# Performance work log

Hardware: AMD Instinct MI355X
Metric: run time of the kernel (lower is better)

The kernel has to match this reference:

```python
import jax, jax.numpy as jnp
import numpy as np
from jax import lax

B, CEN, CDE, H, W = 4, 256, 256, 64, 64   # de is (B,CDE,H,W); en is (B,CEN,2H,2W)
EMB, K, SCALE = 64, 5, 2
DN = ('NCHW', 'OIHW', 'NCHW')


def conv2d(x, w, b=None, pad=0):
    y = lax.conv_general_dilated(x, w, (1, 1), [(pad, pad), (pad, pad)], dimension_numbers=DN)
    return y if b is None else y + b[None, :, None, None]


def up2(x):
    # F.interpolate(scale_factor=2) default mode='nearest'
    return jnp.repeat(jnp.repeat(x, 2, axis=2), 2, axis=3)


def carafe(de, kernels, k, scale):
    # de: (B,C,H,W); kernels: (B,k*k,H*scale,W*scale), softmax-normalized over dim 1
    b, c, h, w = de.shape
    pad = k // 2
    dep = jnp.pad(de, ((0, 0), (0, 0), (pad, pad), (pad, pad)))
    # (B, C, k*k, H, W): all k*k shifted views of de (zero-padded borders)
    patches = jnp.stack([dep[:, :, dy:dy + h, dx:dx + w]
                         for dy in range(k) for dx in range(k)], axis=2)
    # each output pixel (i,j) reuses the window at source (i//scale, j//scale)
    ker = kernels.reshape(b, k * k, h, scale, w, scale)
    out = jnp.einsum('bkhxwy,bckhw->bchxwy', ker, patches)
    return out.reshape(b, c, h * scale, w * scale)


def xavier_uniform(key, shape):
    fan_out = shape[0] * shape[2] * shape[3]
    fan_in = shape[1] * shape[2] * shape[3]
    limit = float(np.sqrt(6.0 / (fan_in + fan_out)))
    return jax.random.uniform(key, shape, jnp.float32, -limit, limit)


def setup_inputs() -> dict:
    key = jax.random.key(0)
    ks = jax.random.split(key, 7)
    return {
        'en': jax.random.normal(ks[0], (B, CEN, 2 * H, 2 * W), jnp.float32),
        'de': jax.random.normal(ks[1], (B, CDE, H, W), jnp.float32),
        'w_gate': xavier_uniform(ks[2], (1, CDE, 1, 1)),
        'b_gate': jnp.zeros((1,), jnp.float32),
        'w_cen': xavier_uniform(ks[3], (EMB, CEN, 1, 1)),
        'b_cen': jnp.zeros((EMB,), jnp.float32),
        'w_cde': xavier_uniform(ks[4], (EMB, CDE, 1, 1)),
        'w_ce': xavier_uniform(ks[5], (K * K, EMB, 3, 3)),
        'b_ce': jnp.zeros((K * K,), jnp.float32),
    }


def reference(en, de, w_gate, b_gate, w_cen, b_cen, w_cde, w_ce, b_ce):
    # GateGenerator: sigmoid(interpolate(conv1x1(de), x2))
    gate = jax.nn.sigmoid(up2(conv2d(de, w_gate, b_gate)))
    # SemiShift: shared 3x3 content encoder on compressed en and upsampled compressed de
    enc = conv2d(en, w_cen, b_cen)
    dec = conv2d(de, w_cde)          # no bias
    logits = conv2d(enc, w_ce, b_ce, pad=1) + up2(conv2d(dec, w_ce, b_ce, pad=1))
    kernels = jax.nn.softmax(logits, axis=1)
    return gate * en + (1.0 - gate) * carafe(de, kernels, K, SCALE)
```

## Files before the change

### kernel.cpp

```cpp
#include <hip/hip_runtime.h>
#include <math.h>

#define BB 4
#define C 256
#define H 64
#define W 64
#define HW 4096
#define HO 128
#define WO 128
#define HWO 16384
#define EMB 64

typedef __bf16 bf16x8 __attribute__((ext_vector_type(8)));
typedef __bf16 bf16x4 __attribute__((ext_vector_type(4)));
typedef float  f32x4  __attribute__((ext_vector_type(4)));

__device__ __forceinline__ f32x4 mfma16(bf16x8 a, bf16x8 b, f32x4 c) {
    return __builtin_amdgcn_mfma_f32_16x16x32_bf16(a, b, c, 0, 0, 0);
}

__global__ void k_prep2(const float* __restrict__ w_cen,
                        const float* __restrict__ w_cde,
                        const float* __restrict__ w_ce,
                        __bf16* __restrict__ wbf_cen,
                        __bf16* __restrict__ wbf_cde,
                        __bf16* __restrict__ w3) {
    const int n1 = EMB * C;
    const int n3 = 9 * 2 * 16 * EMB;
    for (int idx = blockIdx.x * blockDim.x + threadIdx.x; idx < n1;
         idx += gridDim.x * blockDim.x) {
        wbf_cen[idx] = (__bf16)w_cen[idx];
        wbf_cde[idx] = (__bf16)w_cde[idx];
    }
    for (int idx = blockIdx.x * blockDim.x + threadIdx.x; idx < n3;
         idx += gridDim.x * blockDim.x) {
        int e = idx & 63;
        int m = (idx >> 6) & 15;
        int mt = (idx >> 10) & 1;
        int tap = idx >> 11;
        int q = mt * 16 + m;
        int dy = tap / 3, dx = tap % 3;
        w3[idx] = (q < 25) ? (__bf16)w_ce[((q * EMB + e) * 3 + dy) * 3 + dx]
                           : (__bf16)0.0f;
    }
}

__global__ __launch_bounds__(256) void k_gemm1(
        const float* __restrict__ en, const float* __restrict__ de,
        const __bf16* __restrict__ wbf_cen, const __bf16* __restrict__ wbf_cde,
        const float* __restrict__ b_cen,
        __bf16* __restrict__ enc_t, __bf16* __restrict__ dec_t) {
    int t = threadIdx.x;
    int w = t >> 6, lane = t & 63;
    int n = lane & 15, q = lane >> 4;
    bool isenc = blockIdx.x < 512;
    const float* X; const __bf16* Wt; __bf16* Y; int plane, px0;
    if (isenc) {
        int blk = blockIdx.x; int b = blk >> 7; px0 = (blk & 127) << 7;
        X = en + (size_t)b * C * HWO; plane = HWO; Wt = wbf_cen;
        Y = enc_t + (size_t)b * HWO * EMB;
    } else {
        int blk = blockIdx.x - 512; int b = blk >> 5; px0 = (blk & 31) << 7;
        X = de + (size_t)b * C * HW; plane = HW; Wt = wbf_cde;
        Y = dec_t + (size_t)b * HW * EMB;
    }
    int pxw = px0 + w * 32;
    f32x4 acc[4][2] = {};
    for (int kc = 0; kc < 8; kc++) {
        int c0 = kc * 32;
        bf16x8 af[4];
        #pragma unroll
        for (int mt = 0; mt < 4; mt++)
            af[mt] = *(const bf16x8*)(Wt + (mt * 16 + n) * C + c0 + q * 8);
        #pragma unroll
        for (int nt = 0; nt < 2; nt++) {
            int px = pxw + nt * 16 + n;
            bf16x8 bv;
            #pragma unroll
            for (int j = 0; j < 8; j++)
                bv[j] = (__bf16)X[(size_t)(c0 + q * 8 + j) * plane + px];
            #pragma unroll
            for (int mt = 0; mt < 4; mt++)
                acc[mt][nt] = mfma16(af[mt], bv, acc[mt][nt]);
        }
    }
    #pragma unroll
    for (int mt = 0; mt < 4; mt++) {
        int e0 = mt * 16 + q * 4;
        float bias[4];
        #pragma unroll
        for (int r = 0; r < 4; r++) bias[r] = isenc ? b_cen[e0 + r] : 0.f;
        #pragma unroll
        for (int nt = 0; nt < 2; nt++) {
            int px = pxw + nt * 16 + n;
            bf16x4 ov;
            #pragma unroll
            for (int r = 0; r < 4; r++)
                ov[r] = (__bf16)(acc[mt][nt][r] + bias[r]);
            *(bf16x4*)(Y + (size_t)px * EMB + e0) = ov;
        }
    }
}

__global__ __launch_bounds__(256) void k_gate(
        const float* __restrict__ de, const float* __restrict__ w_gate,
        const float* __restrict__ b_gate, float* __restrict__ gate_lr) {
    __shared__ float red[4][64];
    int t = threadIdx.x;
    int px = t & 63, cs = t >> 6;
    int b = blockIdx.x >> 6, p0 = (blockIdx.x & 63) * 64;
    const float* dptr = de + ((size_t)b * C + cs * 64) * HW + p0 + px;
    float s = 0.f;
    #pragma unroll 4
    for (int c = 0; c < 64; c++)
        s += dptr[(size_t)c * HW] * w_gate[cs * 64 + c];
    red[cs][px] = s;
    __syncthreads();
    if (t < 64) {
        float v = red[0][t] + red[1][t] + red[2][t] + red[3][t] + b_gate[0];
        gate_lr[b * HW + p0 + t] = 1.f / (1.f + __expf(-v));
    }
}

__global__ __launch_bounds__(256) void k_conv3m(
        const __bf16* __restrict__ enc_t, const __bf16* __restrict__ dec_t,
        const __bf16* __restrict__ w3, const float* __restrict__ b_ce,
        float* __restrict__ tmp1, float* __restrict__ tmp2) {
    int t = threadIdx.x;
    int w = t >> 6, lane = t & 63;
    int n = lane & 15, q = lane >> 4;
    bool hi = blockIdx.x < 1024;
    const __bf16* src; float* dst; int b, y, width, plane, x;
    if (hi) {
        int blk = blockIdx.x; b = blk >> 8; int r = blk & 255;
        y = r >> 1; int seg = r & 1;
        width = WO; plane = HWO;
        src = enc_t + (size_t)b * HWO * EMB; dst = tmp1;
        x = seg * 64 + w * 16 + n;
    } else {
        int blk = blockIdx.x - 1024; b = blk >> 6; y = blk & 63;
        width = W; plane = HW;
        src = dec_t + (size_t)b * HW * EMB; dst = tmp2;
        x = w * 16 + n;
    }
    f32x4 acc[2] = {};
    bf16x8 bz;
    #pragma unroll
    for (int j = 0; j < 8; j++) bz[j] = (__bf16)0.0f;
    #pragma unroll
    for (int dy = -1; dy <= 1; dy++) {
        int yy = y + dy;
        if ((unsigned)yy >= (unsigned)width) continue;
        #pragma unroll
        for (int dx = -1; dx <= 1; dx++) {
            int tap = (dy + 1) * 3 + (dx + 1);
            int xx = x + dx;
            bool valid = (unsigned)xx < (unsigned)width;
            int xc = valid ? xx : 0;
            const __bf16* brow = src + ((size_t)yy * width + xc) * EMB;
            #pragma unroll
            for (int kc = 0; kc < 2; kc++) {
                bf16x8 bv = *(const bf16x8*)(brow + kc * 32 + q * 8);
                if (!valid) bv = bz;
                #pragma unroll
                for (int mt = 0; mt < 2; mt++) {
                    bf16x8 av = *(const bf16x8*)(
                        w3 + ((tap * 2 + mt) * 16 + n) * EMB + kc * 32 + q * 8);
                    acc[mt] = mfma16(av, bv, acc[mt]);
                }
            }
        }
    }
    #pragma unroll
    for (int mt = 0; mt < 2; mt++) {
        #pragma unroll
        for (int r = 0; r < 4; r++) {
            int m = mt * 16 + q * 4 + r;
            if (m < 25)
                dst[((size_t)(b * 25 + m)) * plane + y * width + x] =
                    acc[mt][r] + b_ce[m];
        }
    }
}

__global__ __launch_bounds__(256) void k_softmax(
        const float* __restrict__ tmp1, const float* __restrict__ tmp2,
        float* __restrict__ kbuf) {
    int gid = blockIdx.x * 256 + threadIdx.x;
    int b = gid >> 14, p = gid & 16383;
    int i = p >> 7, j = p & 127;
    int pl = (i >> 1) * W + (j >> 1);
    float kern[28];
    float m = -1e30f;
    #pragma unroll
    for (int q = 0; q < 25; q++) {
        float l = tmp1[((size_t)(b * 25 + q) << 14) + p]
                + tmp2[((size_t)(b * 25 + q) << 12) + pl];
        kern[q] = l;
        m = fmaxf(m, l);
    }
    float s = 0.f;
    #pragma unroll
    for (int q = 0; q < 25; q++) { kern[q] = __expf(kern[q] - m); s += kern[q]; }
    float inv = 1.f / s;
    #pragma unroll
    for (int q = 0; q < 25; q++) kern[q] *= inv;
    kern[25] = kern[26] = kern[27] = 0.f;
    float4* o = (float4*)(kbuf + (size_t)gid * 28);
    #pragma unroll
    for (int q = 0; q < 7; q++) o[q] = ((float4*)kern)[q];
}

#define NCH 16
__global__ __launch_bounds__(256) void k_final(
        const float* __restrict__ en, const float* __restrict__ de,
        const float* __restrict__ kbuf, const float* __restrict__ gate_lr,
        float* __restrict__ out) {
    __shared__ float sde[NCH][6][36];
    int t = threadIdx.x;
    int tx = t & 63, ty = t >> 6;
    int tileX = blockIdx.x & 1;
    int tileY = blockIdx.x >> 1;
    int c0 = blockIdx.y * NCH;
    int b = blockIdx.z;
    int i0 = tileY * 4, j0 = tileX * 64;
    int yl0 = i0 >> 1, xl0 = j0 >> 1;

    const float* dbase = de + ((size_t)b * C + c0) * HW;
    for (int idx = t; idx < NCH * 216; idx += 256) {
        int c = idx / 216, r = idx % 216;
        int y = r / 36, x = r % 36;
        int yy = yl0 - 2 + y, xx = xl0 - 2 + x;
        float v = 0.f;
        if ((unsigned)yy < (unsigned)H && (unsigned)xx < (unsigned)W)
            v = dbase[(size_t)c * HW + yy * W + xx];
        ((float*)sde)[idx] = v;
    }

    int i = i0 + ty, j = j0 + tx;
    int p = i * WO + j;
    float kern[28];
    const float4* kb = (const float4*)(kbuf + ((size_t)(b * HWO + p)) * 28);
    #pragma unroll
    for (int q = 0; q < 7; q++) ((float4*)kern)[q] = kb[q];
    float g = gate_lr[b * HW + (i >> 1) * W + (j >> 1)];
    __syncthreads();

    int wy = ty >> 1, wx = tx >> 1;
    const float* ebase = en + ((size_t)b * C + c0) * HWO + p;
    float* obase = out + ((size_t)b * C + c0) * HWO + p;
    #pragma unroll 2
    for (int c = 0; c < NCH; c++) {
        float acc = 0.f;
        #pragma unroll
        for (int dy = 0; dy < 5; dy++) {
            #pragma unroll
            for (int dx = 0; dx < 5; dx++)
                acc += kern[dy * 5 + dx] * sde[c][wy + dy][wx + dx];
        }
        float ev = ebase[(size_t)c * HWO];
        obase[(size_t)c * HWO] = g * ev + (1.f - g) * acc;
    }
}

extern "C" void kernel_launch(void* const* d_in, const int* in_sizes, int n_in,
                              void* d_out, int out_size, void* d_ws, size_t ws_size,
                              hipStream_t stream) {
    const float* en     = (const float*)d_in[0];
    const float* de     = (const float*)d_in[1];
    const float* w_gate = (const float*)d_in[2];
    const float* b_gate = (const float*)d_in[3];
    const float* w_cen  = (const float*)d_in[4];
    const float* b_cen  = (const float*)d_in[5];
    const float* w_cde  = (const float*)d_in[6];
    const float* w_ce   = (const float*)d_in[7];
    const float* b_ce   = (const float*)d_in[8];
    float* out = (float*)d_out;

    __bf16* wsb    = (__bf16*)d_ws;
    __bf16* wbf_cen = wsb;
    __bf16* wbf_cde = wbf_cen + 16384;
    __bf16* w3      = wbf_cde + 16384;
    __bf16* enc_t   = w3 + 18432;
    __bf16* dec_t   = enc_t + 4194304;
    float* wsf     = (float*)((char*)d_ws + (size_t)(16384 + 16384 + 18432
                              + 4194304 + 1048576) * 2);
    float* tmp1    = wsf;
    float* tmp2    = tmp1 + 1638400;
    float* gate_lr = tmp2 + 409600;
    float* kbuf    = gate_lr + 16384;

    k_prep2<<<72, 256, 0, stream>>>(w_cen, w_cde, w_ce, wbf_cen, wbf_cde, w3);
    k_gemm1<<<640, 256, 0, stream>>>(en, de, wbf_cen, wbf_cde, b_cen, enc_t, dec_t);
    k_gate<<<256, 256, 0, stream>>>(de, w_gate, b_gate, gate_lr);
    k_conv3m<<<1280, 256, 0, stream>>>(enc_t, dec_t, w3, b_ce, tmp1, tmp2);
    k_softmax<<<256, 256, 0, stream>>>(tmp1, tmp2, kbuf);
    k_final<<<dim3(64, 16, 4), 256, 0, stream>>>(en, de, kbuf, gate_lr, out);
}
```

Measured before the change: 240.0 us.

## Fuse gate into de GEMM, stage conv/GEMM inputs in LDS, retile CARAFE output

The separate gate kernel is removed: the gate 1x1 conv becomes a fifth MFMA row tile in the de projection GEMM, which saves one pass over de. The GEMM now stages input tiles through LDS with float4 loads instead of strided scalar global reads. The 3x3 conv stages a halo of rows in LDS. Softmax splits the 25 taps across four threads per pixel to get more parallelism. The final CARAFE kernel has each thread compute the 2x2 output pixels that share one low-res window, so each shared-memory read serves four outputs, at the cost of more registers.

```diff
diff --git a/kernel.cpp b/kernel.cpp
--- a/kernel.cpp
+++ b/kernel.cpp
@@ -21,18 +21,23 @@
 
 __global__ void k_prep2(const float* __restrict__ w_cen,
                         const float* __restrict__ w_cde,
+                        const float* __restrict__ w_gate,
                         const float* __restrict__ w_ce,
                         __bf16* __restrict__ wbf_cen,
-                        __bf16* __restrict__ wbf_cde,
+                        __bf16* __restrict__ wdec5,
                         __bf16* __restrict__ w3) {
-    const int n1 = EMB * C;
-    const int n3 = 9 * 2 * 16 * EMB;
-    for (int idx = blockIdx.x * blockDim.x + threadIdx.x; idx < n1;
+    for (int idx = blockIdx.x * blockDim.x + threadIdx.x; idx < 16384;
+         idx += gridDim.x * blockDim.x)
+        wbf_cen[idx] = (__bf16)w_cen[idx];
+    for (int idx = blockIdx.x * blockDim.x + threadIdx.x; idx < 20480;
          idx += gridDim.x * blockDim.x) {
-        wbf_cen[idx] = (__bf16)w_cen[idx];
-        wbf_cde[idx] = (__bf16)w_cde[idx];
-    }
-    for (int idx = blockIdx.x * blockDim.x + threadIdx.x; idx < n3;
+        int c = idx & 255, m = (idx >> 8) & 15;
+        float v;
+        if (idx < 16384) v = w_cde[idx];
+        else             v = (m == 0) ? w_gate[c] : 0.f;
+        wdec5[idx] = (__bf16)v;
+    }
+    for (int idx = blockIdx.x * blockDim.x + threadIdx.x; idx < 18432;
          idx += gridDim.x * blockDim.x) {
         int e = idx & 63;
         int m = (idx >> 6) & 15;
@@ -47,121 +52,116 @@
 
 __global__ __launch_bounds__(256) void k_gemm1(
         const float* __restrict__ en, const float* __restrict__ de,
-        const __bf16* __restrict__ wbf_cen, const __bf16* __restrict__ wbf_cde,
-        const float* __restrict__ b_cen,
-        __bf16* __restrict__ enc_t, __bf16* __restrict__ dec_t) {
+        const __bf16* __restrict__ wbf_cen, const __bf16* __restrict__ wdec5,
+        const float* __restrict__ b_cen, const float* __restrict__ b_gate,
+        __bf16* __restrict__ enc_t, __bf16* __restrict__ dec_t,
+        float* __restrict__ gate_lr) {
+    __shared__ float xs[32 * 64];
     int t = threadIdx.x;
     int w = t >> 6, lane = t & 63;
     int n = lane & 15, q = lane >> 4;
-    bool isenc = blockIdx.x < 512;
-    const float* X; const __bf16* Wt; __bf16* Y; int plane, px0;
+    bool isenc = blockIdx.x < 1024;
+    const float* X; const __bf16* Wt; __bf16* Y; int plane, px0, b;
     if (isenc) {
-        int blk = blockIdx.x; int b = blk >> 7; px0 = (blk & 127) << 7;
+        int blk = blockIdx.x; b = blk >> 8; px0 = (blk & 255) << 6;
         X = en + (size_t)b * C * HWO; plane = HWO; Wt = wbf_cen;
         Y = enc_t + (size_t)b * HWO * EMB;
     } else {
-        int blk = blockIdx.x - 512; int b = blk >> 5; px0 = (blk & 31) << 7;
-        X = de + (size_t)b * C * HW; plane = HW; Wt = wbf_cde;
+        int blk = blockIdx.x - 1024; b = blk >> 6; px0 = (blk & 63) << 6;
+        X = de + (size_t)b * C * HW; plane = HW; Wt = wdec5;
         Y = dec_t + (size_t)b * HW * EMB;
     }
-    int pxw = px0 + w * 32;
-    f32x4 acc[4][2] = {};
+    int px = w * 16 + n;
+    f32x4 acc[5] = {};
     for (int kc = 0; kc < 8; kc++) {
         int c0 = kc * 32;
-        bf16x8 af[4];
+        __syncthreads();
+        #pragma unroll
+        for (int i = 0; i < 2; i++) {
+            int idx = i * 256 + t;
+            int c = idx >> 4, p4 = (idx & 15) << 2;
+            float4 v = *(const float4*)(X + (size_t)(c0 + c) * plane + px0 + p4);
+            *(float4*)(xs + c * 64 + p4) = v;
+        }
+        __syncthreads();
+        bf16x8 af[5];
         #pragma unroll
         for (int mt = 0; mt < 4; mt++)
             af[mt] = *(const bf16x8*)(Wt + (mt * 16 + n) * C + c0 + q * 8);
-        #pragma unroll
-        for (int nt = 0; nt < 2; nt++) {
-            int px = pxw + nt * 16 + n;
-            bf16x8 bv;
-            #pragma unroll
-            for (int j = 0; j < 8; j++)
-                bv[j] = (__bf16)X[(size_t)(c0 + q * 8 + j) * plane + px];
-            #pragma unroll
-            for (int mt = 0; mt < 4; mt++)
-                acc[mt][nt] = mfma16(af[mt], bv, acc[mt][nt]);
-        }
-    }
+        if (!isenc)
+            af[4] = *(const bf16x8*)(Wt + (64 + n) * C + c0 + q * 8);
+        bf16x8 bv;
+        #pragma unroll
+        for (int j = 0; j < 8; j++)
+            bv[j] = (__bf16)xs[(q * 8 + j) * 64 + px];
+        #pragma unroll
+        for (int mt = 0; mt < 4; mt++)
+            acc[mt] = mfma16(af[mt], bv, acc[mt]);
+        if (!isenc)
+            acc[4] = mfma16(af[4], bv, acc[4]);
+    }
+    int gpx = px0 + px;
     #pragma unroll
     for (int mt = 0; mt < 4; mt++) {
         int e0 = mt * 16 + q * 4;
-        float bias[4];
-        #pragma unroll
-        for (int r = 0; r < 4; r++) bias[r] = isenc ? b_cen[e0 + r] : 0.f;
-        #pragma unroll
-        for (int nt = 0; nt < 2; nt++) {
-            int px = pxw + nt * 16 + n;
-            bf16x4 ov;
-            #pragma unroll
-            for (int r = 0; r < 4; r++)
-                ov[r] = (__bf16)(acc[mt][nt][r] + bias[r]);
-            *(bf16x4*)(Y + (size_t)px * EMB + e0) = ov;
-        }
-    }
-}
-
-__global__ __launch_bounds__(256) void k_gate(
-        const float* __restrict__ de, const float* __restrict__ w_gate,
-        const float* __restrict__ b_gate, float* __restrict__ gate_lr) {
-    __shared__ float red[4][64];
-    int t = threadIdx.x;
-    int px = t & 63, cs = t >> 6;
-    int b = blockIdx.x >> 6, p0 = (blockIdx.x & 63) * 64;
-    const float* dptr = de + ((size_t)b * C + cs * 64) * HW + p0 + px;
-    float s = 0.f;
-    #pragma unroll 4
-    for (int c = 0; c < 64; c++)
-        s += dptr[(size_t)c * HW] * w_gate[cs * 64 + c];
-    red[cs][px] = s;
-    __syncthreads();
-    if (t < 64) {
-        float v = red[0][t] + red[1][t] + red[2][t] + red[3][t] + b_gate[0];
-        gate_lr[b * HW + p0 + t] = 1.f / (1.f + __expf(-v));
-    }
+        bf16x4 ov;
+        #pragma unroll
+        for (int r = 0; r < 4; r++) {
+            float bias = isenc ? b_cen[e0 + r] : 0.f;
+            ov[r] = (__bf16)(acc[mt][r] + bias);
+        }
+        *(bf16x4*)(Y + (size_t)gpx * EMB + e0) = ov;
+    }
+    if (!isenc && q == 0)
+        gate_lr[b * HW + gpx] = 1.f / (1.f + __expf(-(acc[4][0] + b_gate[0])));
 }
 
 __global__ __launch_bounds__(256) void k_conv3m(
         const __bf16* __restrict__ enc_t, const __bf16* __restrict__ dec_t,
         const __bf16* __restrict__ w3, const float* __restrict__ b_ce,
         float* __restrict__ tmp1, float* __restrict__ tmp2) {
+    __shared__ __bf16 sfr[8 * 3 * 66 * 8];
     int t = threadIdx.x;
     int w = t >> 6, lane = t & 63;
     int n = lane & 15, q = lane >> 4;
     bool hi = blockIdx.x < 1024;
-    const __bf16* src; float* dst; int b, y, width, plane, x;
+    const __bf16* src; float* dst; int b, y, width, plane, x0;
     if (hi) {
         int blk = blockIdx.x; b = blk >> 8; int r = blk & 255;
-        y = r >> 1; int seg = r & 1;
+        y = r >> 1; x0 = (r & 1) * 64;
         width = WO; plane = HWO;
         src = enc_t + (size_t)b * HWO * EMB; dst = tmp1;
-        x = seg * 64 + w * 16 + n;
     } else {
-        int blk = blockIdx.x - 1024; b = blk >> 6; y = blk & 63;
+        int blk = blockIdx.x - 1024; b = blk >> 6; y = blk & 63; x0 = 0;
         width = W; plane = HW;
         src = dec_t + (size_t)b * HW * EMB; dst = tmp2;
-        x = w * 16 + n;
-    }
+    }
+    bf16x8 zf;
+    #pragma unroll
+    for (int j = 0; j < 8; j++) zf[j] = (__bf16)0.0f;
+    for (int idx = t; idx < 1584; idx += 256) {
+        int f = idx & 7;
+        int rem = idx >> 3;
+        int xloc = rem % 66, row = rem / 66;
+        int yy = y + row - 1, xg = x0 - 1 + xloc;
+        bf16x8 v = zf;
+        if ((unsigned)yy < (unsigned)width && (unsigned)xg < (unsigned)width)
+            v = *(const bf16x8*)(src + ((size_t)yy * width + xg) * EMB + f * 8);
+        *(bf16x8*)(sfr + (((f * 3) + row) * 66 + xloc) * 8) = v;
+    }
+    __syncthreads();
+
+    int x = w * 16 + n;
     f32x4 acc[2] = {};
-    bf16x8 bz;
-    #pragma unroll
-    for (int j = 0; j < 8; j++) bz[j] = (__bf16)0.0f;
-    #pragma unroll
-    for (int dy = -1; dy <= 1; dy++) {
-        int yy = y + dy;
-        if ((unsigned)yy >= (unsigned)width) continue;
-        #pragma unroll
-        for (int dx = -1; dx <= 1; dx++) {
-            int tap = (dy + 1) * 3 + (dx + 1);
-            int xx = x + dx;
-            bool valid = (unsigned)xx < (unsigned)width;
-            int xc = valid ? xx : 0;
-            const __bf16* brow = src + ((size_t)yy * width + xc) * EMB;
+    #pragma unroll
+    for (int row = 0; row < 3; row++) {
+        #pragma unroll
+        for (int dx = 0; dx < 3; dx++) {
+            int tap = row * 3 + dx;
             #pragma unroll
             for (int kc = 0; kc < 2; kc++) {
-                bf16x8 bv = *(const bf16x8*)(brow + kc * 32 + q * 8);
-                if (!valid) bv = bz;
+                bf16x8 bv = *(const bf16x8*)(
+                    sfr + ((((kc * 4 + q) * 3) + row) * 66 + x + dx) * 8);
                 #pragma unroll
                 for (int mt = 0; mt < 2; mt++) {
                     bf16x8 av = *(const bf16x8*)(
@@ -177,7 +177,7 @@
         for (int r = 0; r < 4; r++) {
             int m = mt * 16 + q * 4 + r;
             if (m < 25)
-                dst[((size_t)(b * 25 + m)) * plane + y * width + x] =
+                dst[((size_t)(b * 25 + m)) * plane + y * width + x0 + x] =
                     acc[mt][r] + b_ce[m];
         }
     }
@@ -186,80 +186,99 @@
 __global__ __launch_bounds__(256) void k_softmax(
         const float* __restrict__ tmp1, const float* __restrict__ tmp2,
         float* __restrict__ kbuf) {
-    int gid = blockIdx.x * 256 + threadIdx.x;
-    int b = gid >> 14, p = gid & 16383;
+    __shared__ float red[4][64];
+    int t = threadIdx.x;
+    int tx = t & 63, qg = t >> 6;
+    int gp = blockIdx.x * 64 + tx;
+    int b = gp >> 14, p = gp & 16383;
     int i = p >> 7, j = p & 127;
     int pl = (i >> 1) * W + (j >> 1);
-    float kern[28];
-    float m = -1e30f;
-    #pragma unroll
-    for (int q = 0; q < 25; q++) {
-        float l = tmp1[((size_t)(b * 25 + q) << 14) + p]
-                + tmp2[((size_t)(b * 25 + q) << 12) + pl];
-        kern[q] = l;
-        m = fmaxf(m, l);
-    }
+    int q0 = qg * 7;
+    int nq = (qg < 3) ? 7 : 4;
+    float l[7];
+    float mx = -1e30f;
+    for (int iq = 0; iq < nq; iq++) {
+        int qq = q0 + iq;
+        l[iq] = tmp1[((size_t)(b * 25 + qq) << 14) + p]
+              + tmp2[((size_t)(b * 25 + qq) << 12) + pl];
+        mx = fmaxf(mx, l[iq]);
+    }
+    red[qg][tx] = mx;
+    __syncthreads();
+    mx = fmaxf(fmaxf(red[0][tx], red[1][tx]), fmaxf(red[2][tx], red[3][tx]));
     float s = 0.f;
-    #pragma unroll
-    for (int q = 0; q < 25; q++) { kern[q] = __expf(kern[q] - m); s += kern[q]; }
+    for (int iq = 0; iq < nq; iq++) { l[iq] = __expf(l[iq] - mx); s += l[iq]; }
+    __syncthreads();
+    red[qg][tx] = s;
+    __syncthreads();
+    s = red[0][tx] + red[1][tx] + red[2][tx] + red[3][tx];
     float inv = 1.f / s;
-    #pragma unroll
-    for (int q = 0; q < 25; q++) kern[q] *= inv;
-    kern[25] = kern[26] = kern[27] = 0.f;
-    float4* o = (float4*)(kbuf + (size_t)gid * 28);
-    #pragma unroll
-    for (int q = 0; q < 7; q++) o[q] = ((float4*)kern)[q];
-}
-
-#define NCH 16
+    float* kb = kbuf + (size_t)gp * 28;
+    for (int iq = 0; iq < nq; iq++) kb[q0 + iq] = l[iq] * inv;
+    if (qg == 3) { kb[25] = 0.f; kb[26] = 0.f; kb[27] = 0.f; }
+}
+
 __global__ __launch_bounds__(256) void k_final(
         const float* __restrict__ en, const float* __restrict__ de,
         const float* __restrict__ kbuf, const float* __restrict__ gate_lr,
         float* __restrict__ out) {
-    __shared__ float sde[NCH][6][36];
+    __shared__ float sde[16][20][21];
     int t = threadIdx.x;
-    int tx = t & 63, ty = t >> 6;
-    int tileX = blockIdx.x & 1;
-    int tileY = blockIdx.x >> 1;
-    int c0 = blockIdx.y * NCH;
+    int tlx = blockIdx.x & 3, tly = blockIdx.x >> 2;
+    int c0 = blockIdx.y * 16;
     int b = blockIdx.z;
-    int i0 = tileY * 4, j0 = tileX * 64;
-    int yl0 = i0 >> 1, xl0 = j0 >> 1;
+    int y0 = tly * 16, x0 = tlx * 16;
 
     const float* dbase = de + ((size_t)b * C + c0) * HW;
-    for (int idx = t; idx < NCH * 216; idx += 256) {
-        int c = idx / 216, r = idx % 216;
-        int y = r / 36, x = r % 36;
-        int yy = yl0 - 2 + y, xx = xl0 - 2 + x;
+    for (int idx = t; idx < 16 * 400; idx += 256) {
+        int c = idx / 400, rem = idx % 400;
+        int yy0 = rem / 20, xx0 = rem % 20;
+        int yy = y0 - 2 + yy0, xx = x0 - 2 + xx0;
         float v = 0.f;
         if ((unsigned)yy < (unsigned)H && (unsigned)xx < (unsigned)W)
             v = dbase[(size_t)c * HW + yy * W + xx];
-        ((float*)sde)[idx] = v;
-    }
-
-    int i = i0 + ty, j = j0 + tx;
-    int p = i * WO + j;
-    float kern[28];
-    const float4* kb = (const float4*)(kbuf + ((size_t)(b * HWO + p)) * 28);
-    #pragma unroll
-    for (int q = 0; q < 7; q++) ((float4*)kern)[q] = kb[q];
-    float g = gate_lr[b * HW + (i >> 1) * W + (j >> 1)];
-    __syncthreads();
-
-    int wy = ty >> 1, wx = tx >> 1;
-    const float* ebase = en + ((size_t)b * C + c0) * HWO + p;
-    float* obase = out + ((size_t)b * C + c0) * HWO + p;
-    #pragma unroll 2
-    for (int c = 0; c < NCH; c++) {
-        float acc = 0.f;
+        sde[c][yy0][xx0] = v;
+    }
+
+    int ty = t >> 4, tx = t & 15;
+    int yl = y0 + ty, xl = x0 + tx;
+    float4 kf[4][7];
+    #pragma unroll
+    for (int hp = 0; hp < 4; hp++) {
+        int ii = 2 * yl + (hp >> 1), jj = 2 * xl + (hp & 1);
+        const float4* kb = (const float4*)(
+            kbuf + ((size_t)b * HWO + ii * WO + jj) * 28);
+        #pragma unroll
+        for (int v = 0; v < 7; v++) kf[hp][v] = kb[v];
+    }
+    float g = gate_lr[b * HW + yl * W + xl];
+    float gm = 1.f - g;
+    __syncthreads();
+
+    const float* ebase = en + ((size_t)b * C + c0) * HWO;
+    float* obase = out + ((size_t)b * C + c0) * HWO;
+    for (int c = 0; c < 16; c++) {
+        float acc0 = 0.f, acc1 = 0.f, acc2 = 0.f, acc3 = 0.f;
         #pragma unroll
         for (int dy = 0; dy < 5; dy++) {
             #pragma unroll
-            for (int dx = 0; dx < 5; dx++)
-                acc += kern[dy * 5 + dx] * sde[c][wy + dy][wx + dx];
-        }
-        float ev = ebase[(size_t)c * HWO];
-        obase[(size_t)c * HWO] = g * ev + (1.f - g) * acc;
+            for (int dx = 0; dx < 5; dx++) {
+                float v = sde[c][ty + dy][tx + dx];
+                int k = dy * 5 + dx;
+                acc0 += ((const float*)&kf[0][0])[k] * v;
+                acc1 += ((const float*)&kf[1][0])[k] * v;
+                acc2 += ((const float*)&kf[2][0])[k] * v;
+                acc3 += ((const float*)&kf[3][0])[k] * v;
+            }
+        }
+        size_t cc = (size_t)c * HWO;
+        float2 e0 = *(const float2*)(ebase + cc + (2 * yl) * WO + 2 * xl);
+        float2 e1 = *(const float2*)(ebase + cc + (2 * yl + 1) * WO + 2 * xl);
+        float2 o0, o1;
+        o0.x = g * e0.x + gm * acc0;  o0.y = g * e0.y + gm * acc1;
+        o1.x = g * e1.x + gm * acc2;  o1.y = g * e1.y + gm * acc3;
+        *(float2*)(obase + cc + (2 * yl) * WO + 2 * xl) = o0;
+        *(float2*)(obase + cc + (2 * yl + 1) * WO + 2 * xl) = o1;
     }
 }
 
@@ -277,23 +296,24 @@
     const float* b_ce   = (const float*)d_in[8];
     float* out = (float*)d_out;
 
-    __bf16* wsb    = (__bf16*)d_ws;
+    __bf16* wsb     = (__bf16*)d_ws;
     __bf16* wbf_cen = wsb;
-    __bf16* wbf_cde = wbf_cen + 16384;
-    __bf16* w3      = wbf_cde + 16384;
+    __bf16* wdec5   = wbf_cen + 16384;
+    __bf16* w3      = wdec5 + 20480;
     __bf16* enc_t   = w3 + 18432;
     __bf16* dec_t   = enc_t + 4194304;
-    float* wsf     = (float*)((char*)d_ws + (size_t)(16384 + 16384 + 18432
+    float* wsf     = (float*)((char*)d_ws + (size_t)(16384 + 20480 + 18432
                               + 4194304 + 1048576) * 2);
     float* tmp1    = wsf;
     float* tmp2    = tmp1 + 1638400;
     float* gate_lr = tmp2 + 409600;
     float* kbuf    = gate_lr + 16384;
 
-    k_prep2<<<72, 256, 0, stream>>>(w_cen, w_cde, w_ce, wbf_cen, wbf_cde, w3);
-    k_gemm1<<<640, 256, 0, stream>>>(en, de, wbf_cen, wbf_cde, b_cen, enc_t, dec_t);
-    k_gate<<<256, 256, 0, stream>>>(de, w_gate, b_gate, gate_lr);
+    k_prep2<<<80, 256, 0, stream>>>(w_cen, w_cde, w_gate, w_ce,
+                                    wbf_cen, wdec5, w3);
+    k_gemm1<<<1280, 256, 0, stream>>>(en, de, wbf_cen, wdec5, b_cen, b_gate,
+                                      enc_t, dec_t, gate_lr);
     k_conv3m<<<1280, 256, 0, stream>>>(enc_t, dec_t, w3, b_ce, tmp1, tmp2);
-    k_softmax<<<256, 256, 0, stream>>>(tmp1, tmp2, kbuf);
-    k_final<<<dim3(64, 16, 4), 256, 0, stream>>>(en, de, kbuf, gate_lr, out);
-}
+    k_softmax<<<1024, 256, 0, stream>>>(tmp1, tmp2, kbuf);
+    k_final<<<dim3(16, 16, 4), 256, 0, stream>>>(en, de, kbuf, gate_lr, out);
+}
```

New measurement: 241.1 us. Within noise of the previous version (+0.5%).
